# Optimization experiments

Hardware: AMD Instinct MI355X
Metric: run time of the kernel (lower is better)

The kernel has to match this reference:

```python
import jax, jax.numpy as jnp
import numpy as np

N = 50000          # num vertices
K = 16             # max padded neighbors
D = 256            # feature dim
H = 256            # num_hidddens


def setup_inputs() -> dict:
    key = jax.random.key(0)
    k1, k2, k3, k4, k5 = jax.random.split(key, 5)
    vertex_feat = jax.random.normal(k1, (N, D), dtype=jnp.float32)
    neighbors_idx = jax.random.randint(k2, (N, K), 0, N, dtype=jnp.int32)
    valid_lens = jax.random.randint(k3, (N,), 0, K + 1, dtype=jnp.int32)
    W = jax.random.normal(k4, (D, H), dtype=jnp.float32) * (1.0 / np.sqrt(D))
    B = jax.random.normal(k5, (D, H), dtype=jnp.float32) * (1.0 / np.sqrt(D))
    return {"vertex_feat": vertex_feat, "neighbors_idx": neighbors_idx,
            "valid_lens": valid_lens, "W": W, "B": B}


def reference(vertex_feat, neighbors_idx, valid_lens, W, B):
    # gather neighbor features: [N, K, D]
    nb = vertex_feat[neighbors_idx]
    # sequence mask over padded neighbor slots: [N, K]
    mask = (jnp.arange(K)[None, :] < valid_lens[:, None]).astype(vertex_feat.dtype)
    # masked sum then mean (valid_lens==0 -> divide by 1, matching tf.where guard)
    agg = jnp.einsum('nkd,nk->nd', nb, mask)
    denom = jnp.maximum(valid_lens, 1).astype(vertex_feat.dtype)
    agg = agg / denom[:, None]
    # dual dense (no bias) + relu
    out = jax.nn.relu(agg @ W + vertex_feat @ B)
    return out
```

## Files before the change

kernel.cpp:

```cpp
#include <hip/hip_runtime.h>
#include <stdint.h>


#define N_V   50000
#define KNB   16
#define D_F   256
#define H_F   256
#define HK2   512
#define NPAD  50048

typedef __bf16 bf16x8 __attribute__((ext_vector_type(8)));
typedef float  f32x4  __attribute__((ext_vector_type(4)));
typedef float  f32x8  __attribute__((ext_vector_type(8)));
typedef unsigned short ushort8 __attribute__((ext_vector_type(8)));

static __device__ __forceinline__ unsigned short f2bf(float f) {
    union { float f; unsigned u; } v; v.f = f;
    unsigned u = v.u;
    u += 0x7fffu + ((u >> 16) & 1u);
    return (unsigned short)(u >> 16);
}
static __device__ __forceinline__ float bf2f(unsigned short u) {
    union { unsigned u; float f; } v; v.u = ((unsigned)u) << 16; return v.f;
}
static __device__ __forceinline__ void load16(const void* g, void* l) {
    __builtin_amdgcn_global_load_lds(
        (__attribute__((address_space(1))) void*)g,
        (__attribute__((address_space(3))) void*)l, 16, 0, 0);
}

__global__ __launch_bounds__(256) void vf_convert(
    const float* __restrict__ vf, unsigned short* __restrict__ vfb) {
    const int total = NPAD * (D_F / 8);
    for (int c = blockIdx.x * 256 + threadIdx.x; c < total; c += gridDim.x * 256) {
        int n = c >> 5;
        int off = (c & 31) * 8;
        ushort8 o;
        if (n < N_V) {
            const float4 a = *(const float4*)(vf + (size_t)n * D_F + off);
            const float4 b = *(const float4*)(vf + (size_t)n * D_F + off + 4);
            o[0]=f2bf(a.x); o[1]=f2bf(a.y); o[2]=f2bf(a.z); o[3]=f2bf(a.w);
            o[4]=f2bf(b.x); o[5]=f2bf(b.y); o[6]=f2bf(b.z); o[7]=f2bf(b.w);
        } else {
            o = (ushort8)(0);
        }
        *(ushort8*)(vfb + (size_t)n * D_F + off) = o;
    }
}

__global__ __launch_bounds__(256) void wbt_convert(
    const float* __restrict__ W, const float* __restrict__ Bm,
    unsigned short* __restrict__ WBt) {
    __shared__ unsigned short t[32][33];
    const int k0 = blockIdx.x * 32;
    const int h0 = blockIdx.y * 32;
    const int tid = threadIdx.x;
    {
        int r  = tid >> 3;
        int c4 = (tid & 7) * 4;
        const float* src = (h0 < 256)
            ? (W  + (size_t)(k0 + r) * H_F + h0 + c4)
            : (Bm + (size_t)(k0 + r) * H_F + (h0 - 256) + c4);
        float4 v = *(const float4*)src;
        t[r][c4 + 0] = f2bf(v.x); t[r][c4 + 1] = f2bf(v.y);
        t[r][c4 + 2] = f2bf(v.z); t[r][c4 + 3] = f2bf(v.w);
    }
    __syncthreads();
    {
        int hh  = tid >> 3;
        int kk4 = (tid & 7) * 4;
        ushort4 o;
        o.x = t[kk4 + 0][hh]; o.y = t[kk4 + 1][hh];
        o.z = t[kk4 + 2][hh]; o.w = t[kk4 + 3][hh];
        *(ushort4*)(WBt + (size_t)(h0 + hh) * D_F + k0 + kk4) = o;
    }
}

__global__ __launch_bounds__(512, 4) void gemm_y(
    const unsigned short* __restrict__ vfb,
    const unsigned short* __restrict__ WBt,
    unsigned short* __restrict__ Y) {
    __shared__ char Bp[65536];
    __shared__ char Ap[2][8192];
    const int bn = blockIdx.x * 128;
    const int bm = blockIdx.y * 128;
    const int tid = threadIdx.x;
    const int wave = tid >> 6, lane = tid & 63;
    const int wm = wave & 3, wn = wave >> 2;

    f32x4 acc[2][4];
    const f32x4 fzero = {0.f, 0.f, 0.f, 0.f};
#pragma unroll
    for (int i = 0; i < 2; ++i)
#pragma unroll
        for (int j = 0; j < 4; ++j) acc[i][j] = fzero;

#pragma unroll
    for (int i = 0; i < 8; ++i) {
        unsigned P = i * 8192u + tid * 16u;
        unsigned r = P >> 9, pc = P & 511u;
        unsigned lc = pc ^ ((r & 7u) << 4);
        load16((const char*)WBt + (size_t)(bn + r) * 512 + lc,
               Bp + i * 8192 + wave * 1024);
    }
    auto stageA = [&](int buf, int t) {
        unsigned P = tid * 16u;
        unsigned r = P >> 6, pc = P & 63u;
        unsigned lc = pc ^ ((r & 3u) << 4);
        load16((const char*)vfb + (size_t)(bm + r) * 512 + t * 64 + lc,
               Ap[buf] + wave * 1024);
    };
    stageA(0, 0);
    __syncthreads();

    int cur = 0;
    for (int t = 0; t < 8; ++t) {
        if (t < 7) stageA(cur ^ 1, t + 1);
        bf16x8 af[2], bfr[4];
#pragma unroll
        for (int mf = 0; mf < 2; ++mf) {
            unsigned r = wm * 32u + mf * 16u + (lane & 15);
            unsigned c = ((unsigned)lane >> 4) << 4;
            af[mf] = *(const bf16x8*)(Ap[cur] + r * 64 + (c ^ ((r & 3u) << 4)));
        }
#pragma unroll
        for (int nf = 0; nf < 4; ++nf) {
            unsigned r = wn * 64u + nf * 16u + (lane & 15);
            unsigned c = t * 64u + (((unsigned)lane >> 4) << 4);
            bfr[nf] = *(const bf16x8*)(Bp + r * 512 + (c ^ ((r & 7u) << 4)));
        }
#pragma unroll
        for (int mf = 0; mf < 2; ++mf)
#pragma unroll
            for (int nf = 0; nf < 4; ++nf)
                acc[mf][nf] = __builtin_amdgcn_mfma_f32_16x16x32_bf16(
                    af[mf], bfr[nf], acc[mf][nf], 0, 0, 0);
        __syncthreads();
        cur ^= 1;
    }

#pragma unroll
    for (int mf = 0; mf < 2; ++mf) {
        int row0 = bm + wm * 32 + mf * 16 + ((lane >> 4) << 2);
#pragma unroll
        for (int nf = 0; nf < 4; ++nf) {
            int col = bn + wn * 64 + nf * 16 + (lane & 15);
            f32x4 v = acc[mf][nf];
#pragma unroll
            for (int i = 0; i < 4; ++i)
                Y[(size_t)(row0 + i) * HK2 + col] = f2bf(v[i]);
        }
    }
}

__global__ __launch_bounds__(256) void gather_out(
    const unsigned short* __restrict__ Y, const int* __restrict__ nbr,
    const int* __restrict__ lens, float* __restrict__ out) {
    const int wave = threadIdx.x >> 6;
    const int lane = threadIdx.x & 63;
    const int half = lane >> 5, laneh = lane & 31;
    const int v = blockIdx.x * 8 + wave * 2 + half;
    const int base = lane & 32;
    const int col = laneh * 8;

    const int len = lens[v];
    const int idx = nbr[(size_t)v * KNB + (laneh & 15)];
    const ushort8 y2 = *(const ushort8*)(Y + (size_t)v * HK2 + 256 + col);

    f32x8 acc = {0.f,0.f,0.f,0.f,0.f,0.f,0.f,0.f};
#define ROW_(j) (*(const ushort8*)(Y + (size_t)(j) * HK2 + col))
#define ACC_(r) { acc[0]+=bf2f(r[0]); acc[1]+=bf2f(r[1]); acc[2]+=bf2f(r[2]); \
                  acc[3]+=bf2f(r[3]); acc[4]+=bf2f(r[4]); acc[5]+=bf2f(r[5]); \
                  acc[6]+=bf2f(r[6]); acc[7]+=bf2f(r[7]); }
    int k = 0;
    for (; k + 4 <= len; k += 4) {
        int j0 = __shfl(idx, base + k),     j1 = __shfl(idx, base + k + 1);
        int j2 = __shfl(idx, base + k + 2), j3 = __shfl(idx, base + k + 3);
        ushort8 r0 = ROW_(j0), r1 = ROW_(j1), r2 = ROW_(j2), r3 = ROW_(j3);
        ACC_(r0); ACC_(r1); ACC_(r2); ACC_(r3);
    }
    for (; k < len; ++k) {
        int j = __shfl(idx, base + k);
        ushort8 r = ROW_(j);
        ACC_(r);
    }
#undef ROW_
#undef ACC_
    const float inv = 1.0f / (float)(len > 0 ? len : 1);
    float4 o0, o1;
    o0.x = fmaxf(fmaf(acc[0], inv, bf2f(y2[0])), 0.f);
    o0.y = fmaxf(fmaf(acc[1], inv, bf2f(y2[1])), 0.f);
    o0.z = fmaxf(fmaf(acc[2], inv, bf2f(y2[2])), 0.f);
    o0.w = fmaxf(fmaf(acc[3], inv, bf2f(y2[3])), 0.f);
    o1.x = fmaxf(fmaf(acc[4], inv, bf2f(y2[4])), 0.f);
    o1.y = fmaxf(fmaf(acc[5], inv, bf2f(y2[5])), 0.f);
    o1.z = fmaxf(fmaf(acc[6], inv, bf2f(y2[6])), 0.f);
    o1.w = fmaxf(fmaf(acc[7], inv, bf2f(y2[7])), 0.f);
    float* op = out + (size_t)v * H_F + col;
    *(float4*)op = o0;
    *(float4*)(op + 4) = o1;
}

extern "C" void kernel_launch(void* const* d_in, const int* in_sizes, int n_in,
                              void* d_out, int out_size, void* d_ws, size_t ws_size,
                              hipStream_t stream) {
    const float* vf   = (const float*)d_in[0];
    const int*   nbr  = (const int*)d_in[1];
    const int*   lens = (const int*)d_in[2];
    const float* W    = (const float*)d_in[3];
    const float* Bm   = (const float*)d_in[4];
    float* out = (float*)d_out;

    unsigned short* Y    = (unsigned short*)d_ws;
    unsigned short* vfb  = Y + (size_t)NPAD * HK2;
    unsigned short* WBt  = vfb + (size_t)NPAD * D_F;

    hipLaunchKernelGGL(vf_convert, dim3(2048), dim3(256), 0, stream, vf, vfb);
    hipLaunchKernelGGL(wbt_convert, dim3(8, 16), dim3(256), 0, stream, W, Bm, WBt);
    hipLaunchKernelGGL(gemm_y, dim3(4, NPAD / 128), dim3(512), 0, stream,
                       vfb, WBt, Y);
    hipLaunchKernelGGL(gather_out, dim3(N_V / 8), dim3(256), 0, stream,
                       Y, nbr, lens, out);
}
```

Measured before the change: 174.1 us.

## Fuse fp32-to-bf16 conversion of vertex features into GEMM A-tile staging

Removes the separate vf_convert kernel and its bf16 intermediate buffer. The GEMM now loads fp32 vertex features into registers, converts them to bf16 and writes them into swizzled LDS, double-buffered across k-steps. This saves a full write and re-read of a bf16 copy of the features plus one kernel launch. In exchange, each of the 4 column blocks reads the fp32 A rows from global memory and converts them again, and the asynchronous LDS-direct loads become register-staged loads. Rows past N are clamped to the last valid row.

After: 173.6 us. About the same (-0.2%).

```diff
diff --git a/kernel.cpp b/kernel.cpp
--- a/kernel.cpp
+++ b/kernel.cpp
@@ -27,25 +27,6 @@
     __builtin_amdgcn_global_load_lds(
         (__attribute__((address_space(1))) void*)g,
         (__attribute__((address_space(3))) void*)l, 16, 0, 0);
-}
-
-__global__ __launch_bounds__(256) void vf_convert(
-    const float* __restrict__ vf, unsigned short* __restrict__ vfb) {
-    const int total = NPAD * (D_F / 8);
-    for (int c = blockIdx.x * 256 + threadIdx.x; c < total; c += gridDim.x * 256) {
-        int n = c >> 5;
-        int off = (c & 31) * 8;
-        ushort8 o;
-        if (n < N_V) {
-            const float4 a = *(const float4*)(vf + (size_t)n * D_F + off);
-            const float4 b = *(const float4*)(vf + (size_t)n * D_F + off + 4);
-            o[0]=f2bf(a.x); o[1]=f2bf(a.y); o[2]=f2bf(a.z); o[3]=f2bf(a.w);
-            o[4]=f2bf(b.x); o[5]=f2bf(b.y); o[6]=f2bf(b.z); o[7]=f2bf(b.w);
-        } else {
-            o = (ushort8)(0);
-        }
-        *(ushort8*)(vfb + (size_t)n * D_F + off) = o;
-    }
 }
 
 __global__ __launch_bounds__(256) void wbt_convert(
@@ -77,7 +58,7 @@
 }
 
 __global__ __launch_bounds__(512, 4) void gemm_y(
-    const unsigned short* __restrict__ vfb,
+    const float* __restrict__ vf,
     const unsigned short* __restrict__ WBt,
     unsigned short* __restrict__ Y) {
     __shared__ char Bp[65536];
@@ -103,19 +84,31 @@
         load16((const char*)WBt + (size_t)(bn + r) * 512 + lc,
                Bp + i * 8192 + wave * 1024);
     }
-    auto stageA = [&](int buf, int t) {
-        unsigned P = tid * 16u;
-        unsigned r = P >> 6, pc = P & 63u;
-        unsigned lc = pc ^ ((r & 3u) << 4);
-        load16((const char*)vfb + (size_t)(bm + r) * 512 + t * 64 + lc,
-               Ap[buf] + wave * 1024);
+
+    const int ar = tid >> 2;
+    const int ak = (tid & 3) * 8;
+    const int arow_g = (bm + ar < N_V) ? bm + ar : N_V - 1;
+    const float* aptr = vf + (size_t)arow_g * D_F + ak;
+    const unsigned aOff = ar * 64u + (((unsigned)(ak * 2)) ^ (((unsigned)ar & 3u) << 4));
+    float4 a0, a1;
+    auto loadA = [&](int t) {
+        a0 = *(const float4*)(aptr + t * 32);
+        a1 = *(const float4*)(aptr + t * 32 + 4);
     };
-    stageA(0, 0);
+    auto writeA = [&](int buf) {
+        ushort8 o;
+        o[0]=f2bf(a0.x); o[1]=f2bf(a0.y); o[2]=f2bf(a0.z); o[3]=f2bf(a0.w);
+        o[4]=f2bf(a1.x); o[5]=f2bf(a1.y); o[6]=f2bf(a1.z); o[7]=f2bf(a1.w);
+        *(ushort8*)(Ap[buf] + aOff) = o;
+    };
+
+    loadA(0);
+    writeA(0);
     __syncthreads();
 
     int cur = 0;
     for (int t = 0; t < 8; ++t) {
-        if (t < 7) stageA(cur ^ 1, t + 1);
+        if (t < 7) loadA(t + 1);
         bf16x8 af[2], bfr[4];
 #pragma unroll
         for (int mf = 0; mf < 2; ++mf) {
@@ -135,6 +128,7 @@
             for (int nf = 0; nf < 4; ++nf)
                 acc[mf][nf] = __builtin_amdgcn_mfma_f32_16x16x32_bf16(
                     af[mf], bfr[nf], acc[mf][nf], 0, 0, 0);
+        if (t < 7) writeA(cur ^ 1);
         __syncthreads();
         cur ^= 1;
     }
@@ -211,14 +205,12 @@
     const float* Bm   = (const float*)d_in[4];
     float* out = (float*)d_out;
 
-    unsigned short* Y    = (unsigned short*)d_ws;
-    unsigned short* vfb  = Y + (size_t)NPAD * HK2;
-    unsigned short* WBt  = vfb + (size_t)NPAD * D_F;
-
-    hipLaunchKernelGGL(vf_convert, dim3(2048), dim3(256), 0, stream, vf, vfb);
+    unsigned short* Y   = (unsigned short*)d_ws;
+    unsigned short* WBt = Y + (size_t)NPAD * HK2;
+
     hipLaunchKernelGGL(wbt_convert, dim3(8, 16), dim3(256), 0, stream, W, Bm, WBt);
     hipLaunchKernelGGL(gemm_y, dim3(4, NPAD / 128), dim3(512), 0, stream,
-                       vfb, WBt, Y);
+                       vf, WBt, Y);
     hipLaunchKernelGGL(gather_out, dim3(N_V / 8), dim3(256), 0, stream,
                        Y, nbr, lens, out);
 }
```
